# Kernel optimization log

Measured on AMD Instinct MI355X. Metric: run time of the kernel, lower is better.

The kernel has to match this reference:

```python
import jax, jax.numpy as jnp
import numpy as np

B, F, H, P, L, A = 8192, 512, 1024, 64, 32, 16


def setup_inputs() -> dict:
    key = jax.random.key(0)
    ks = jax.random.split(key, 7)
    s = lambda k, shape, fan: jax.random.normal(k, shape, jnp.float32) / np.sqrt(fan)
    return {
        "state": jax.random.normal(ks[0], (B, F), jnp.float32),
        "W0": s(ks[1], (A, H, F), F),
        "b0": jnp.zeros((A, H), jnp.float32),
        "W1": s(ks[2], (A, H, H), H),
        "b1": jnp.zeros((A, H), jnp.float32),
        "W2": s(ks[3], (A, P, H), H),
        "ltl_corr": jax.random.normal(ks[4], (A, P), jnp.float32),
        # learned policies = {0..31}; active-only experts = policies 32..47
        "learned_idx": jnp.arange(L, dtype=jnp.int64),
        "active_idx": jnp.arange(L, L + A, dtype=jnp.int64),
    }


def reference(state, W0, b0, W1, b1, W2, ltl_corr, learned_idx, active_idx):
    # Batched over the A active experts (original loops in Python per expert).
    h = jax.nn.relu(jnp.einsum('bf,ahf->abh', state, W0) + b0[:, None, :])   # [A,B,H]
    h = jax.nn.relu(jnp.einsum('abh,agh->abg', h, W1) + b1[:, None, :])      # [A,B,H]
    x = jnp.einsum('abh,aph->abp', h, W2) + ltl_corr[:, None, :]             # [A,B,P]
    # softmax restricted to learned columns, scattered back into zeros
    sub = jax.nn.softmax(x[:, :, learned_idx], axis=-1)                       # [A,B,L]
    emb = jnp.zeros_like(x).at[:, :, learned_idx].set(sub)                    # [A,B,P]
    # all_emb starts as identity per batch element; active rows replaced
    all_emb = jnp.broadcast_to(jnp.eye(P, dtype=state.dtype), (state.shape[0], P, P))
    all_emb = all_emb.at[:, active_idx, :].set(jnp.transpose(emb, (1, 0, 2)))
    return all_emb
```

## Files before the change

kernel.cpp:

```cpp
#include <hip/hip_runtime.h>
#include <hip/hip_bf16.h>


typedef short v8s __attribute__((ext_vector_type(8)));
typedef float v4f __attribute__((ext_vector_type(4)));
using bf16 = __hip_bfloat16;

#define AS_GLOBAL __attribute__((address_space(1)))
#define AS_LDS    __attribute__((address_space(3)))

static constexpr int Mtot = 8192;
static constexpr int Fdim = 512;
static constexpr int Hdim = 1024;
static constexpr int Pdim = 64;
static constexpr int Aexp = 16;

__device__ __forceinline__ void gload_lds16(const void* g, void* l) {
  __builtin_amdgcn_global_load_lds((const AS_GLOBAL void*)g, (AS_LDS void*)l, 16, 0, 0);
}
__device__ __forceinline__ unsigned short bfu(float x) {
  bf16 h = __float2bfloat16(x);
  return *(unsigned short*)&h;
}
#define MFMA16(d, a, b) d = __builtin_amdgcn_mfma_f32_16x16x32_bf16(a, b, d, 0, 0, 0)
#define WAIT_VM6 asm volatile("s_waitcnt vmcnt(6)" ::: "memory")
#define WAIT_VM0 asm volatile("s_waitcnt vmcnt(0)" ::: "memory")
#define BAR() __builtin_amdgcn_s_barrier()

__device__ __forceinline__ void cvt_span(const float* __restrict__ src,
                                         unsigned short* __restrict__ dst, int n4,
                                         int gid, int nthr) {
  for (int i = gid; i < n4; i += nthr) {
    float4 v = ((const float4*)src)[i];
    ushort4 u;
    u.x = bfu(v.x); u.y = bfu(v.y); u.z = bfu(v.z); u.w = bfu(v.w);
    ((ushort4*)dst)[i] = u;
  }
}

__global__ void cvt_all_kernel(const float* __restrict__ s0, unsigned short* __restrict__ d0, int n0,
                               const float* __restrict__ s1, unsigned short* __restrict__ d1, int n1,
                               const float* __restrict__ s2, unsigned short* __restrict__ d2, int n2,
                               const float* __restrict__ s3, unsigned short* __restrict__ d3, int n3) {
  int gid = blockIdx.x * blockDim.x + threadIdx.x;
  int nthr = gridDim.x * blockDim.x;
  cvt_span(s0, d0, n0, gid, nthr);
  cvt_span(s1, d1, n1, gid, nthr);
  cvt_span(s2, d2, n2, gid, nthr);
  cvt_span(s3, d3, n3, gid, nthr);
}

__global__ void ident_kernel(float* __restrict__ outp, const int* __restrict__ aidx) {
  unsigned long long act = 0;
#pragma unroll
  for (int i = 0; i < Aexp; ++i) act |= 1ull << (aidx[i] & 63);
  const long total4 = (long)Mtot * Pdim * Pdim / 4;
  long i = blockIdx.x * 256 + threadIdx.x;
  const long stride = (long)gridDim.x * 256;
  for (; i < total4; i += stride) {
    long e = i * 4;
    int q = (int)(e & 63);
    int p = (int)((e >> 6) & 63);
    if ((act >> p) & 1) continue;
    v4f v;
    v[0] = (p == q) ? 1.f : 0.f;
    v[1] = (p == q + 1) ? 1.f : 0.f;
    v[2] = (p == q + 2) ? 1.f : 0.f;
    v[3] = (p == q + 3) ? 1.f : 0.f;
    __builtin_nontemporal_store(v, (v4f*)&outp[e]);
  }
}

template <int NT>
__global__ __launch_bounds__(256) void gemm97_kernel(
    const bf16* __restrict__ Ain, long aAmul,
    const bf16* __restrict__ Bw,
    const float* __restrict__ bias,
    bf16* __restrict__ Cout, long aCmul, int nbm) {
  constexpr int K = NT * 64;
  __shared__ short ls[2][128 * 64];
  short* lsA = ls[0];
  short* lsB = ls[1];
  const int t = threadIdx.x;
  const int nwg = nbm * 128;

  const int flat = blockIdx.x;
  const int perx = nwg >> 3;
  const int swz = (flat & 7) * perx + (flat >> 3);
  const int perg = nbm * 8;
  const int g = swz / perg;
  const int e = swz % perg;
  const int msup = e >> 5;
  const int ny = (e >> 2) & 7;
  const int mloc = e & 3;
  const int mBase = (msup * 4 + mloc) * 128;
  const int nBase = ny * 128;

  const bf16* A0 = Ain + (size_t)g * aAmul;
  const bf16* B0 = Bw + (size_t)g * (1024 * K);
  const float* biasE = bias + g * 1024 + nBase;
  bf16* C0 = Cout + (size_t)g * aCmul + nBase;

  const int w = t >> 6, lane = t & 63;
  const int wm = w >> 1, wn = w & 1;
  const int lr = lane & 15, lk = lane >> 4;

  v4f acc[4][4];
#pragma unroll
  for (int m = 0; m < 4; ++m)
#pragma unroll
    for (int n = 0; n < 4; ++n) acc[m][n] = (v4f)(0.f);

  const int rowA = t >> 3;
  const int sg = (t & 7) ^ (rowA & 7);
  const bf16* gA = A0 + (size_t)(mBase + rowA) * K + sg * 8;
  const bf16* gB = B0 + (size_t)(nBase + rowA) * K + sg * 8;

  for (int k0 = 0; k0 < K; k0 += 64) {
#pragma unroll
    for (int i = 0; i < 4; ++i) {
      gload_lds16(gA + (size_t)(i * 32) * K + k0, &lsA[i * 2048 + t * 8]);
      gload_lds16(gB + (size_t)(i * 32) * K + k0, &lsB[i * 2048 + t * 8]);
    }
    __syncthreads();
#pragma unroll
    for (int kk = 0; kk < 2; ++kk) {
      v8s af[4], bfr[4];
#pragma unroll
      for (int m = 0; m < 4; ++m) {
        const int row = wm * 64 + m * 16 + lr;
        af[m] = *(const v8s*)&lsA[row * 64 + ((((kk << 2) + lk) ^ (row & 7)) << 3)];
      }
#pragma unroll
      for (int n = 0; n < 4; ++n) {
        const int row = wn * 64 + n * 16 + lr;
        bfr[n] = *(const v8s*)&lsB[row * 64 + ((((kk << 2) + lk) ^ (row & 7)) << 3)];
      }
#pragma unroll
      for (int m = 0; m < 4; ++m)
#pragma unroll
        for (int n = 0; n < 4; ++n)
          MFMA16(acc[m][n], af[m], bfr[n]);
    }
    __syncthreads();
  }

  unsigned short* wbuf = (unsigned short*)&ls[0][0] + w * 4096;
#pragma unroll
  for (int n = 0; n < 4; ++n) {
    const float bv = biasE[wn * 64 + n * 16 + lr];
#pragma unroll
    for (int m = 0; m < 4; ++m) {
#pragma unroll
      for (int j = 0; j < 4; ++j) {
        const int rl = m * 16 + lk * 4 + j;
        const int cl = n * 16 + lr;
        float v = acc[m][n][j] + bv;
        v = v > 0.f ? v : 0.f;
        wbuf[rl * 64 + (((cl >> 3) ^ (rl & 7)) << 3) + (cl & 7)] = bfu(v);
      }
    }
  }
  const int rr = lane >> 3, gg = lane & 7;
#pragma unroll
  for (int r8 = 0; r8 < 8; ++r8) {
    const int rl = r8 * 8 + rr;
    v8s pk = *(const v8s*)&wbuf[rl * 64 + ((gg ^ (rl & 7)) << 3)];
    const int row = mBase + wm * 64 + rl;
    *(v8s*)&C0[(size_t)row * 1024 + wn * 64 + gg * 8] = pk;
  }
}

__global__ __launch_bounds__(256) void gemm2_softmax_kernel(
    const bf16* __restrict__ h1, const bf16* __restrict__ W2b,
    const float* __restrict__ ltl, const int* __restrict__ lidx,
    const int* __restrict__ aidx, float* __restrict__ outp, int mGlobBase, int MC) {
  __shared__ char smem[49152];
  __shared__ int s_lidx[32];
  __shared__ int s_inv[64];
  __shared__ int s_arow;
  short* lsA = (short*)smem;
  short* lsB = (short*)(smem + 32768);
  float(*X)[68] = (float(*)[68])smem;

  const int aLoc = blockIdx.y;
  const bf16* Ain = h1 + (size_t)aLoc * MC * Hdim;
  const bf16* Bw = W2b + (size_t)aLoc * Pdim * Hdim;
  const float* ltlE = ltl + (size_t)aLoc * Pdim;

  const int t = threadIdx.x;
  const int mBase = blockIdx.x * 128;
  const int w = t >> 6, lane = t & 63;
  const int lr = lane & 15, lk = lane >> 4;
  const int wm = w;

  if (t < 64) s_inv[t] = -1;
  __syncthreads();
  if (t < 32) {
    int q = lidx[t];
    s_lidx[t] = q;
    s_inv[q] = t;
  }
  if (t == 0) s_arow = aidx[aLoc];
  __syncthreads();

  const int srow = t >> 3;
  const int sg = (t & 7) ^ (srow & 7);
  const bf16* gA = Ain + (size_t)(mBase + srow) * Hdim + sg * 8;
  const bf16* gB = Bw + (size_t)srow * Hdim + sg * 8;

  auto stage = [&](int buf, int kt) {
#pragma unroll
    for (int i = 0; i < 4; ++i)
      gload_lds16(gA + (size_t)(i * 32) * Hdim + kt * 64, &lsA[buf * 8192 + i * 2048 + t * 8]);
#pragma unroll
    for (int i = 0; i < 2; ++i)
      gload_lds16(gB + (size_t)(i * 32) * Hdim + kt * 64, &lsB[buf * 4096 + i * 2048 + t * 8]);
  };

  v4f acc[2][4];
#pragma unroll
  for (int m = 0; m < 2; ++m)
#pragma unroll
    for (int n = 0; n < 4; ++n) acc[m][n] = (v4f)(0.f);

  stage(0, 0);
  for (int kt = 0; kt < 16; ++kt) {
    const int buf = kt & 1;
    if (kt + 1 < 16) { stage(buf ^ 1, kt + 1); WAIT_VM6; } else { WAIT_VM0; }
    BAR();
#pragma unroll
    for (int ks = 0; ks < 2; ++ks) {
      v8s af[2], bfr[4];
#pragma unroll
      for (int m = 0; m < 2; ++m) {
        const int row = wm * 32 + m * 16 + lr;
        af[m] = *(const v8s*)&lsA[buf * 8192 + row * 64 + ((((ks << 2) + lk) ^ (lr & 7)) << 3)];
      }
#pragma unroll
      for (int n = 0; n < 4; ++n) {
        const int row = n * 16 + lr;
        bfr[n] = *(const v8s*)&lsB[buf * 4096 + row * 64 + ((((ks << 2) + lk) ^ (lr & 7)) << 3)];
      }
#pragma unroll
      for (int m = 0; m < 2; ++m)
#pragma unroll
        for (int n = 0; n < 4; ++n)
          MFMA16(acc[m][n], af[m], bfr[n]);
    }
    BAR();
  }

#pragma unroll
  for (int n = 0; n < 4; ++n) {
    const int col = n * 16 + lr;
    const float lc = ltlE[col];
#pragma unroll
    for (int m = 0; m < 2; ++m)
#pragma unroll
      for (int j = 0; j < 4; ++j)
        X[wm * 32 + m * 16 + lk * 4 + j][col] = acc[m][n][j] + lc;
  }
  __syncthreads();

  if (t < 128) {
    const int r = t;
    float mx = -1e30f;
#pragma unroll
    for (int l = 0; l < 32; ++l) mx = fmaxf(mx, X[r][s_lidx[l]]);
    float s = 0.f;
#pragma unroll
    for (int l = 0; l < 32; ++l) s += __expf(X[r][s_lidx[l]] - mx);
    const float rs = 1.f / s;
    const size_t obase = ((size_t)(mGlobBase + mBase + r) * 64 + s_arow) * 64;
#pragma unroll
    for (int q0 = 0; q0 < 64; q0 += 4) {
      v4f v;
      v[0] = (s_inv[q0 + 0] >= 0) ? __expf(X[r][q0 + 0] - mx) * rs : 0.f;
      v[1] = (s_inv[q0 + 1] >= 0) ? __expf(X[r][q0 + 1] - mx) * rs : 0.f;
      v[2] = (s_inv[q0 + 2] >= 0) ? __expf(X[r][q0 + 2] - mx) * rs : 0.f;
      v[3] = (s_inv[q0 + 3] >= 0) ? __expf(X[r][q0 + 3] - mx) * rs : 0.f;
      __builtin_nontemporal_store(v, (v4f*)&outp[obase + q0]);
    }
  }
}

extern "C" void kernel_launch(void* const* d_in, const int* in_sizes, int n_in,
                              void* d_out, int out_size, void* d_ws, size_t ws_size,
                              hipStream_t stream) {
  const float* state = (const float*)d_in[0];
  const float* W0 = (const float*)d_in[1];
  const float* b0 = (const float*)d_in[2];
  const float* W1 = (const float*)d_in[3];
  const float* b1 = (const float*)d_in[4];
  const float* W2 = (const float*)d_in[5];
  const float* ltl = (const float*)d_in[6];
  const int* lidx = (const int*)d_in[7];
  const int* aidx = (const int*)d_in[8];
  float* outp = (float*)d_out;

  char* ws = (char*)d_ws;
  bf16* stateb = (bf16*)ws;
  bf16* W0b = stateb + (size_t)Mtot * Fdim;
  bf16* W1b = W0b + (size_t)Aexp * Hdim * Fdim;
  bf16* W2b = W1b + (size_t)Aexp * Hdim * Hdim;
  bf16* h0 = W2b + (size_t)Aexp * Pdim * Hdim;
  const size_t fixedB = (size_t)(Mtot * Fdim + Aexp * Hdim * Fdim +
                                 Aexp * Hdim * Hdim + Aexp * Pdim * Hdim) * 2;
  int MC = 2048;
  while (MC > 512 && fixedB + (size_t)2 * Aexp * MC * Hdim * 2 + 4096 > ws_size) MC >>= 1;
  bf16* h1 = h0 + (size_t)Aexp * MC * Hdim;

  ident_kernel<<<dim3(4096), dim3(256), 0, stream>>>(outp, aidx);
  cvt_all_kernel<<<dim3(2048), dim3(256), 0, stream>>>(
      state, (unsigned short*)stateb, Mtot * Fdim / 4,
      W0, (unsigned short*)W0b, Aexp * Hdim * Fdim / 4,
      W1, (unsigned short*)W1b, Aexp * Hdim * Hdim / 4,
      W2, (unsigned short*)W2b, Aexp * Pdim * Hdim / 4);

  const int nbm = MC / 128;
  for (int mOff = 0; mOff < Mtot; mOff += MC) {
    gemm97_kernel<Fdim / 64><<<dim3(nbm * 128), dim3(256), 0, stream>>>(
        stateb + (size_t)mOff * Fdim, 0L,
        W0b, b0, h0, (long)MC * Hdim, nbm);
    gemm97_kernel<Hdim / 64><<<dim3(nbm * 128), dim3(256), 0, stream>>>(
        h0, (long)MC * Hdim,
        W1b, b1, h1, (long)MC * Hdim, nbm);
    gemm2_softmax_kernel<<<dim3(MC / 128, Aexp), dim3(256), 0, stream>>>(
        h1, W2b, ltl, lidx, aidx, outp, mOff, MC);
  }
}
```

Baseline: 688.7 us.

## Fuse second hidden GEMM with output GEMM and softmax to skip h1 round-trip

Layer-1 GEMM, layer-2 GEMM and softmax now run in one kernel. Each workgroup owns 128 rows of one expert and loops over eight 128-column tiles of H, keeping each ReLU'd h1 tile in LDS and feeding it straight into the W2 projection. This removes the h1 global write and read, drops one kernel launch, and lets MC grow because only h0 needs workspace. In exchange each workgroup does far more serial work with fewer workgroups, staging is no longer double-buffered, W2 is read directly from global memory, and gemm97's LDS-staged coalesced epilogue becomes scalar bf16 stores.

New measurement: 921.9 us. 33.9% more time.

```diff
diff --git a/kernel.cpp b/kernel.cpp
--- a/kernel.cpp
+++ b/kernel.cpp
@@ -23,8 +23,6 @@
   return *(unsigned short*)&h;
 }
 #define MFMA16(d, a, b) d = __builtin_amdgcn_mfma_f32_16x16x32_bf16(a, b, d, 0, 0, 0)
-#define WAIT_VM6 asm volatile("s_waitcnt vmcnt(6)" ::: "memory")
-#define WAIT_VM0 asm volatile("s_waitcnt vmcnt(0)" ::: "memory")
 #define BAR() __builtin_amdgcn_s_barrier()
 
 __device__ __forceinline__ void cvt_span(const float* __restrict__ src,
@@ -78,9 +76,8 @@
     const float* __restrict__ bias,
     bf16* __restrict__ Cout, long aCmul, int nbm) {
   constexpr int K = NT * 64;
-  __shared__ short ls[2][128 * 64];
-  short* lsA = ls[0];
-  short* lsB = ls[1];
+  __shared__ short lsA[128 * 64];
+  __shared__ short lsB[128 * 64];
   const int t = threadIdx.x;
   const int nwg = nbm * 128;
 
@@ -145,54 +142,43 @@
     __syncthreads();
   }
 
-  unsigned short* wbuf = (unsigned short*)&ls[0][0] + w * 4096;
 #pragma unroll
   for (int n = 0; n < 4; ++n) {
-    const float bv = biasE[wn * 64 + n * 16 + lr];
+    const int colIn = wn * 64 + n * 16 + lr;
+    const float bv = biasE[colIn];
 #pragma unroll
     for (int m = 0; m < 4; ++m) {
+      const int row0 = mBase + wm * 64 + m * 16 + lk * 4;
 #pragma unroll
       for (int j = 0; j < 4; ++j) {
-        const int rl = m * 16 + lk * 4 + j;
-        const int cl = n * 16 + lr;
         float v = acc[m][n][j] + bv;
         v = v > 0.f ? v : 0.f;
-        wbuf[rl * 64 + (((cl >> 3) ^ (rl & 7)) << 3) + (cl & 7)] = bfu(v);
-      }
-    }
-  }
-  const int rr = lane >> 3, gg = lane & 7;
-#pragma unroll
-  for (int r8 = 0; r8 < 8; ++r8) {
-    const int rl = r8 * 8 + rr;
-    v8s pk = *(const v8s*)&wbuf[rl * 64 + ((gg ^ (rl & 7)) << 3)];
-    const int row = mBase + wm * 64 + rl;
-    *(v8s*)&C0[(size_t)row * 1024 + wn * 64 + gg * 8] = pk;
-  }
-}
-
-__global__ __launch_bounds__(256) void gemm2_softmax_kernel(
-    const bf16* __restrict__ h1, const bf16* __restrict__ W2b,
-    const float* __restrict__ ltl, const int* __restrict__ lidx,
-    const int* __restrict__ aidx, float* __restrict__ outp, int mGlobBase, int MC) {
-  __shared__ char smem[49152];
+        C0[(size_t)(row0 + j) * 1024 + colIn] = __float2bfloat16(v);
+      }
+    }
+  }
+}
+
+__global__ __launch_bounds__(256) void fused23_kernel(
+    const bf16* __restrict__ h0, long aAmul,
+    const bf16* __restrict__ W1b, const float* __restrict__ b1,
+    const bf16* __restrict__ W2b, const float* __restrict__ ltl,
+    const int* __restrict__ lidx, const int* __restrict__ aidx,
+    float* __restrict__ outp, int mGlobBase, int nbm) {
+  __shared__ short lsA[128 * 64];
+  __shared__ short lsB[128 * 64];
+  __shared__ char uni[128 * 68 * 4];
   __shared__ int s_lidx[32];
   __shared__ int s_inv[64];
   __shared__ int s_arow;
-  short* lsA = (short*)smem;
-  short* lsB = (short*)(smem + 32768);
-  float(*X)[68] = (float(*)[68])smem;
-
-  const int aLoc = blockIdx.y;
-  const bf16* Ain = h1 + (size_t)aLoc * MC * Hdim;
-  const bf16* Bw = W2b + (size_t)aLoc * Pdim * Hdim;
-  const float* ltlE = ltl + (size_t)aLoc * Pdim;
 
   const int t = threadIdx.x;
-  const int mBase = blockIdx.x * 128;
-  const int w = t >> 6, lane = t & 63;
-  const int lr = lane & 15, lk = lane >> 4;
-  const int wm = w;
+  const int nwg = nbm * Aexp;
+  const int flat = blockIdx.x;
+  const int perx = nwg >> 3;
+  const int swz = (flat & 7) * perx + (flat >> 3);
+  const int g = swz / nbm;
+  const int mBase = (swz % nbm) * 128;
 
   if (t < 64) s_inv[t] = -1;
   __syncthreads();
@@ -201,56 +187,115 @@
     s_lidx[t] = q;
     s_inv[q] = t;
   }
-  if (t == 0) s_arow = aidx[aLoc];
-  __syncthreads();
+  if (t == 0) s_arow = aidx[g];
+
+  const int w = t >> 6, lane = t & 63;
+  const int wm = w;
+  const int lr = lane & 15, lk = lane >> 4;
+
+  const bf16* A0 = h0 + (size_t)g * aAmul;
+  const bf16* W1g = W1b + (size_t)g * (Hdim * Hdim);
+  const bf16* W2g = W2b + (size_t)g * (Pdim * Hdim);
+  const float* b1g = b1 + g * Hdim;
+  const float* ltlE = ltl + g * Pdim;
 
   const int srow = t >> 3;
   const int sg = (t & 7) ^ (srow & 7);
-  const bf16* gA = Ain + (size_t)(mBase + srow) * Hdim + sg * 8;
-  const bf16* gB = Bw + (size_t)srow * Hdim + sg * 8;
-
-  auto stage = [&](int buf, int kt) {
-#pragma unroll
-    for (int i = 0; i < 4; ++i)
-      gload_lds16(gA + (size_t)(i * 32) * Hdim + kt * 64, &lsA[buf * 8192 + i * 2048 + t * 8]);
-#pragma unroll
-    for (int i = 0; i < 2; ++i)
-      gload_lds16(gB + (size_t)(i * 32) * Hdim + kt * 64, &lsB[buf * 4096 + i * 2048 + t * 8]);
+  const bf16* gA = A0 + (size_t)(mBase + srow) * Hdim + sg * 8;
+  const bf16* gBW = W1g + (size_t)srow * Hdim + sg * 8;
+
+  auto stage = [&](int ntile, int kt) {
+#pragma unroll
+    for (int i = 0; i < 4; ++i) {
+      gload_lds16(gA + (size_t)(i * 32) * Hdim + kt * 64, &lsA[i * 2048 + t * 8]);
+      gload_lds16(gBW + (size_t)(ntile * 128 + i * 32) * Hdim + kt * 64,
+                  &lsB[i * 2048 + t * 8]);
+    }
   };
 
-  v4f acc[2][4];
+  unsigned short* h1t = (unsigned short*)uni + w * 4096;
+  float(*X)[68] = (float(*)[68])uni;
+
+  v4f xac[2][4];
 #pragma unroll
   for (int m = 0; m < 2; ++m)
 #pragma unroll
-    for (int n = 0; n < 4; ++n) acc[m][n] = (v4f)(0.f);
+    for (int n = 0; n < 4; ++n) xac[m][n] = (v4f)(0.f);
 
   stage(0, 0);
-  for (int kt = 0; kt < 16; ++kt) {
-    const int buf = kt & 1;
-    if (kt + 1 < 16) { stage(buf ^ 1, kt + 1); WAIT_VM6; } else { WAIT_VM0; }
-    BAR();
-#pragma unroll
-    for (int ks = 0; ks < 2; ++ks) {
-      v8s af[2], bfr[4];
+
+  for (int ntile = 0; ntile < 8; ++ntile) {
+    v4f acc2[2][8];
+#pragma unroll
+    for (int m = 0; m < 2; ++m)
+#pragma unroll
+      for (int n = 0; n < 8; ++n) acc2[m][n] = (v4f)(0.f);
+
+    for (int kt = 0; kt < 16; ++kt) {
+      __syncthreads();
+#pragma unroll
+      for (int ks = 0; ks < 2; ++ks) {
+        v8s af[2], bfr[8];
+#pragma unroll
+        for (int m = 0; m < 2; ++m) {
+          const int row = wm * 32 + m * 16 + lr;
+          af[m] = *(const v8s*)&lsA[row * 64 + ((((ks << 2) + lk) ^ (row & 7)) << 3)];
+        }
+#pragma unroll
+        for (int n = 0; n < 8; ++n) {
+          const int row = n * 16 + lr;
+          bfr[n] = *(const v8s*)&lsB[row * 64 + ((((ks << 2) + lk) ^ (row & 7)) << 3)];
+        }
+#pragma unroll
+        for (int m = 0; m < 2; ++m)
+#pragma unroll
+          for (int n = 0; n < 8; ++n)
+            MFMA16(acc2[m][n], af[m], bfr[n]);
+      }
+      __syncthreads();
+      if (kt < 15) stage(ntile, kt + 1);
+      else if (ntile < 7) stage(ntile + 1, 0);
+    }
+
+#pragma unroll
+    for (int n = 0; n < 8; ++n) {
+      const int col = n * 16 + lr;
+      const float bv = b1g[ntile * 128 + col];
 #pragma unroll
       for (int m = 0; m < 2; ++m) {
-        const int row = wm * 32 + m * 16 + lr;
-        af[m] = *(const v8s*)&lsA[buf * 8192 + row * 64 + ((((ks << 2) + lk) ^ (lr & 7)) << 3)];
-      }
-#pragma unroll
-      for (int n = 0; n < 4; ++n) {
-        const int row = n * 16 + lr;
-        bfr[n] = *(const v8s*)&lsB[buf * 4096 + row * 64 + ((((ks << 2) + lk) ^ (lr & 7)) << 3)];
-      }
+#pragma unroll
+        for (int j = 0; j < 4; ++j) {
+          const int row = m * 16 + lk * 4 + j;
+          float v = acc2[m][n][j] + bv;
+          v = v > 0.f ? v : 0.f;
+          h1t[row * 128 + ((((col >> 3) ^ (row & 7)) << 3) | (col & 7))] = bfu(v);
+        }
+      }
+    }
+    asm volatile("s_waitcnt lgkmcnt(0)" ::: "memory");
+    __builtin_amdgcn_sched_barrier(0);
+
+#pragma unroll
+    for (int ks = 0; ks < 4; ++ks) {
+      v8s a3[2], b3[4];
+#pragma unroll
+      for (int m = 0; m < 2; ++m) {
+        const int row = m * 16 + lr;
+        a3[m] = *(const v8s*)&h1t[row * 128 + ((((ks << 2) + lk) ^ (row & 7)) << 3)];
+      }
+#pragma unroll
+      for (int n = 0; n < 4; ++n)
+        b3[n] = *(const v8s*)&W2g[(size_t)(n * 16 + lr) * Hdim + ntile * 128 +
+                                  ks * 32 + lk * 8];
 #pragma unroll
       for (int m = 0; m < 2; ++m)
 #pragma unroll
         for (int n = 0; n < 4; ++n)
-          MFMA16(acc[m][n], af[m], bfr[n]);
-    }
-    BAR();
-  }
-
+          MFMA16(xac[m][n], a3[m], b3[n]);
+    }
+  }
+
+  __syncthreads();
 #pragma unroll
   for (int n = 0; n < 4; ++n) {
     const int col = n * 16 + lr;
@@ -259,7 +304,7 @@
     for (int m = 0; m < 2; ++m)
 #pragma unroll
       for (int j = 0; j < 4; ++j)
-        X[wm * 32 + m * 16 + lk * 4 + j][col] = acc[m][n][j] + lc;
+        X[wm * 32 + m * 16 + lk * 4 + j][col] = xac[m][n][j] + lc;
   }
   __syncthreads();
 
@@ -307,9 +352,8 @@
   bf16* h0 = W2b + (size_t)Aexp * Pdim * Hdim;
   const size_t fixedB = (size_t)(Mtot * Fdim + Aexp * Hdim * Fdim +
                                  Aexp * Hdim * Hdim + Aexp * Pdim * Hdim) * 2;
-  int MC = 2048;
-  while (MC > 512 && fixedB + (size_t)2 * Aexp * MC * Hdim * 2 + 4096 > ws_size) MC >>= 1;
-  bf16* h1 = h0 + (size_t)Aexp * MC * Hdim;
+  int MC = 4096;
+  while (MC > 512 && fixedB + (size_t)Aexp * MC * Hdim * 2 + 4096 > ws_size) MC >>= 1;
 
   ident_kernel<<<dim3(4096), dim3(256), 0, stream>>>(outp, aidx);
   cvt_all_kernel<<<dim3(2048), dim3(256), 0, stream>>>(
@@ -323,10 +367,7 @@
     gemm97_kernel<Fdim / 64><<<dim3(nbm * 128), dim3(256), 0, stream>>>(
         stateb + (size_t)mOff * Fdim, 0L,
         W0b, b0, h0, (long)MC * Hdim, nbm);
-    gemm97_kernel<Hdim / 64><<<dim3(nbm * 128), dim3(256), 0, stream>>>(
-        h0, (long)MC * Hdim,
-        W1b, b1, h1, (long)MC * Hdim, nbm);
-    gemm2_softmax_kernel<<<dim3(MC / 128, Aexp), dim3(256), 0, stream>>>(
-        h1, W2b, ltl, lidx, aidx, outp, mOff, MC);
-  }
-}
+    fused23_kernel<<<dim3(nbm * Aexp), dim3(256), 0, stream>>>(
+        h0, (long)MC * Hdim, W1b, b1, W2b, ltl, lidx, aidx, outp, mOff, nbm);
+  }
+}
```
